# Performance work log

Measured on AMD Instinct MI355X. Metric: run time of the kernel, lower is better.

## Reference

```python
import jax, jax.numpy as jnp
import numpy as np

NUM_HEADS = 12
HEAD_SIZE = 64
N_EMBED = 768
SEQ_LEN = 2048
BATCH = 4


def setup_inputs() -> dict:
    key = jax.random.key(0)
    ks = jax.random.split(key, 7)
    s = 0.02
    x = jax.random.normal(ks[0], (BATCH, SEQ_LEN, N_EMBED), dtype=jnp.float32)
    # per-head bias-free q/k/v projections: [H, E, D]
    Wq = jax.random.normal(ks[1], (NUM_HEADS, N_EMBED, HEAD_SIZE), dtype=jnp.float32) * s
    Wk = jax.random.normal(ks[2], (NUM_HEADS, N_EMBED, HEAD_SIZE), dtype=jnp.float32) * s
    Wv = jax.random.normal(ks[3], (NUM_HEADS, N_EMBED, HEAD_SIZE), dtype=jnp.float32) * s
    # output projection: Linear(num_heads*head_size, n_embed)
    Wp = jax.random.normal(ks[4], (NUM_HEADS * HEAD_SIZE, N_EMBED), dtype=jnp.float32) * s
    bp = jax.random.normal(ks[5], (N_EMBED,), dtype=jnp.float32) * s
    return {"x": x, "Wq": Wq, "Wk": Wk, "Wv": Wv, "Wp": Wp, "bp": bp}


def reference(x, Wq, Wk, Wv, Wp, bp):
    B, S, E = x.shape
    scale = HEAD_SIZE ** -0.5
    # project all heads at once: [B,H,S,D]
    q = jnp.einsum("bse,hed->bhsd", x, Wq)
    k = jnp.einsum("bse,hed->bhsd", x, Wk)
    v = jnp.einsum("bse,hed->bhsd", x, Wv)
    # scaled dot-product scores [B,H,S,S] with causal mask
    scores = jnp.einsum("bhsd,bhtd->bhst", q, k) * scale
    causal = jnp.tril(jnp.ones((S, S), dtype=bool))
    scores = jnp.where(causal[None, None, :, :], scores, jnp.finfo(scores.dtype).min)
    attn = jax.nn.softmax(scores, axis=-1)
    out = jnp.einsum("bhst,bhtd->bhsd", attn, v)
    # concat heads along feature dim: [B,S,H*D]
    out = out.transpose(0, 2, 1, 3).reshape(B, S, NUM_HEADS * HEAD_SIZE)
    # final projection (dropout rate = 0.0)
    return out @ Wp + bp
```

## Files before the change

kernel.cpp:

```cpp
#include <hip/hip_runtime.h>
#include <hip/hip_bf16.h>


typedef __attribute__((ext_vector_type(8))) short bf16x8;
typedef __attribute__((ext_vector_type(4))) float f32x4;
typedef __attribute__((ext_vector_type(16))) float f32x16;
typedef __attribute__((ext_vector_type(4))) uint u32x4;

#define OFF_WT   6291456
#define OFF_WPT  8060928
#define OFF_QKV  8650752
#define OFF_AO   27525120

#define SCALE_LOG2E 0.1803368801111204f

__device__ inline ushort f2bf(float f) {
  __hip_bfloat16 h = __float2bfloat16(f);
  return *reinterpret_cast<ushort*>(&h);
}
__device__ inline uint cvt_pk(float lo, float hi) {
  uint r;
  asm("v_cvt_pk_bf16_f32 %0, %1, %2" : "=v"(r) : "v"(lo), "v"(hi));
  return r;
}

__global__ __launch_bounds__(256) void transpose_w(const float* __restrict__ src,
                                                   ushort* __restrict__ dst,
                                                   int Edim, int Ddim) {
  __shared__ ushort tile[64][130];
  int mat = blockIdx.y;
  int ntd = Ddim >> 6;
  int te = blockIdx.x / ntd, td = blockIdx.x % ntd;
  size_t base = (size_t)mat * Edim * Ddim;
  int t = threadIdx.x;
#pragma unroll
  for (int i = 0; i < 16; i++) {
    int idx = i * 256 + t;
    int r = idx >> 6, c = idx & 63;
    tile[r][c] = f2bf(src[base + (size_t)(te * 64 + r) * Ddim + td * 64 + c]);
  }
  __syncthreads();
#pragma unroll
  for (int i = 0; i < 16; i++) {
    int idx = i * 256 + t;
    int c = idx >> 6, r = idx & 63;
    dst[base + (size_t)(td * 64 + c) * Edim + te * 64 + r] = tile[r][c];
  }
}

__global__ __launch_bounds__(256) void gemm_qkv(const float* __restrict__ X,
                                                const ushort* __restrict__ Wt,
                                                ushort* __restrict__ qkv,
                                                uint* __restrict__ vtg) {
  __shared__ ushort Alds[128 * 40];
  __shared__ ushort Blds[64 * 40];
  int mb = blockIdx.x, nb = blockIdx.y;
  int t = threadIdx.x, w = t >> 6, lane = t & 63, lo = lane & 15, g = lane >> 4;
  const ushort* Wb = Wt + (size_t)nb * 49152;
  f32x4 acc[2][4];
#pragma unroll
  for (int qi = 0; qi < 2; qi++)
#pragma unroll
    for (int n = 0; n < 4; n++) acc[qi][n] = (f32x4){0.f, 0.f, 0.f, 0.f};
  int r = t >> 2, c4 = t & 3;
  for (int e0 = 0; e0 < 768; e0 += 32) {
#pragma unroll
    for (int i = 0; i < 2; i++) {
      const float* src = &X[(size_t)(mb * 128 + i * 64 + r) * 768 + e0 + c4 * 8];
      float4 f0 = *(const float4*)src;
      float4 f1 = *(const float4*)(src + 4);
      u32x4 pk = {cvt_pk(f0.x, f0.y), cvt_pk(f0.z, f0.w),
                  cvt_pk(f1.x, f1.y), cvt_pk(f1.z, f1.w)};
      *(bf16x8*)&Alds[(i * 64 + r) * 40 + c4 * 8] = __builtin_bit_cast(bf16x8, pk);
    }
    *(bf16x8*)&Blds[r * 40 + c4 * 8] =
        *(const bf16x8*)&Wb[(size_t)r * 768 + e0 + c4 * 8];
    __syncthreads();
    bf16x8 a0 = *(const bf16x8*)&Alds[(w * 32 + lo) * 40 + g * 8];
    bf16x8 a1 = *(const bf16x8*)&Alds[(w * 32 + 16 + lo) * 40 + g * 8];
#pragma unroll
    for (int n = 0; n < 4; n++) {
      bf16x8 b = *(const bf16x8*)&Blds[(n * 16 + lo) * 40 + g * 8];
      acc[0][n] = __builtin_amdgcn_mfma_f32_16x16x32_bf16(a0, b, acc[0][n], 0, 0, 0);
      acc[1][n] = __builtin_amdgcn_mfma_f32_16x16x32_bf16(a1, b, acc[1][n], 0, 0, 0);
    }
    __syncthreads();
  }
  int ty = nb / 12, h = nb % 12;
  if (ty < 2) {
#pragma unroll
    for (int qi = 0; qi < 2; qi++)
#pragma unroll
      for (int n = 0; n < 4; n++) {
        int d = n * 16 + lo;
#pragma unroll
        for (int rr = 0; rr < 4; rr++) {
          int m = mb * 128 + w * 32 + qi * 16 + g * 4 + rr;
          int b = m >> 11, s = m & 2047;
          qkv[(size_t)ty * 6291456 + (size_t)(b * 12 + h) * 131072 + (size_t)s * 64 + d] =
              f2bf(acc[qi][n][rr]);
        }
      }
  } else {
#pragma unroll
    for (int qi = 0; qi < 2; qi++)
#pragma unroll
      for (int n = 0; n < 4; n++) {
        int d = n * 16 + lo;
#pragma unroll
        for (int rr = 0; rr < 4; rr += 2) {
          int m = mb * 128 + w * 32 + qi * 16 + g * 4 + rr;
          int b = m >> 11, s = m & 2047;
          uint pk = cvt_pk(acc[qi][n][rr], acc[qi][n][rr + 1]);
          vtg[(size_t)(b * 12 + h) * 65536 + (s >> 6) * 2048 + d * 32 + ((s & 63) >> 1)] = pk;
        }
      }
  }
}

__global__ __launch_bounds__(256, 3) void attn_fwd(const ushort* __restrict__ Qg,
                                                   const ushort* __restrict__ Kg,
                                                   const uint* __restrict__ Vtg,
                                                   ushort* __restrict__ ao) {
  __shared__ ushort Ksh[2][64 * 72];
  __shared__ uint Vsh[2][64 * 36];
  int x = blockIdx.x;
  int head = x % 48;
  int qb = 15 - x / 48;
  int T = 2 * qb + 2;
  int t = threadIdx.x, w = t >> 6, q31 = t & 31, hi = (t & 63) >> 5;
  const ushort* Q = Qg + (size_t)head * 131072;
  const ushort* K = Kg + (size_t)head * 131072;
  const uint* V = Vtg + (size_t)head * 65536;
  int qstart = qb * 128 + 32 * w;
  int qg = qstart + q31;
  bf16x8 qf[4];
#pragma unroll
  for (int s = 0; s < 4; s++)
    qf[s] = *(const bf16x8*)&Q[(size_t)qg * 64 + s * 16 + hi * 8];
  bf16x8 ones;
#pragma unroll
  for (int i = 0; i < 8; i++) ones[i] = (short)0x3F80;
  f32x16 oacc[2], lacc;
#pragma unroll
  for (int r = 0; r < 16; r++) { oacc[0][r] = 0.f; oacc[1][r] = 0.f; lacc[r] = 0.f; }
  int sr = t >> 3, sc = t & 7;
  bf16x8 kreg[2];
  u32x4 vreg[2];
#pragma unroll
  for (int i = 0; i < 2; i++) {
    kreg[i] = *(const bf16x8*)&K[(size_t)(i * 32 + sr) * 64 + sc * 8];
    vreg[i] = *(const u32x4*)&V[(i * 32 + sr) * 32 + sc * 4];
  }
#pragma unroll
  for (int i = 0; i < 2; i++) {
    *(bf16x8*)&Ksh[0][(i * 32 + sr) * 72 + sc * 8] = kreg[i];
    *(u32x4*)&Vsh[0][(i * 32 + sr) * 36 + sc * 4] = vreg[i];
  }
  for (int kb = 0; kb < T; kb++) {
    __syncthreads();
    if (kb + 1 < T) {
      int t1 = (kb + 1) * 64;
#pragma unroll
      for (int i = 0; i < 2; i++) {
        kreg[i] = *(const bf16x8*)&K[(size_t)(t1 + i * 32 + sr) * 64 + sc * 8];
        vreg[i] = *(const u32x4*)&V[(kb + 1) * 2048 + (i * 32 + sr) * 32 + sc * 4];
      }
    }
    int t0 = kb * 64;
    if (t0 <= qstart + 31) {
      const ushort* Kb = Ksh[kb & 1];
      const uint* Vb = Vsh[kb & 1];
      bool act1 = (t0 + 32 <= qstart + 31);
      f32x16 st0, st1;
#pragma unroll
      for (int r = 0; r < 16; r++) { st0[r] = 0.f; st1[r] = 0.f; }
#pragma unroll
      for (int s = 0; s < 4; s++) {
        bf16x8 kf = *(const bf16x8*)&Kb[q31 * 72 + s * 16 + hi * 8];
        st0 = __builtin_amdgcn_mfma_f32_32x32x16_bf16(kf, qf[s], st0, 0, 0, 0);
      }
      if (act1) {
#pragma unroll
        for (int s = 0; s < 4; s++) {
          bf16x8 kf = *(const bf16x8*)&Kb[(32 + q31) * 72 + s * 16 + hi * 8];
          st1 = __builtin_amdgcn_mfma_f32_32x32x16_bf16(kf, qf[s], st1, 0, 0, 0);
        }
      }
      if (t0 + 31 > qstart) {
        int base = t0 - qstart;
#pragma unroll
        for (int r = 0; r < 16; r++) {
          int crow = (r & 3) + 8 * (r >> 2) + 4 * hi;
          if (base + crow > q31) st0[r] = -3e38f;
        }
      }
      if (act1 && (t0 + 63 > qstart)) {
        int base = t0 + 32 - qstart;
#pragma unroll
        for (int r = 0; r < 16; r++) {
          int crow = (r & 3) + 8 * (r >> 2) + 4 * hi;
          if (base + crow > q31) st1[r] = -3e38f;
        }
      }
#pragma unroll
      for (int r = 0; r < 16; r++)
        st0[r] = __builtin_amdgcn_exp2f(st0[r] * SCALE_LOG2E);
      if (act1) {
#pragma unroll
        for (int r = 0; r < 16; r++)
          st1[r] = __builtin_amdgcn_exp2f(st1[r] * SCALE_LOG2E);
      }
      int ns = act1 ? 4 : 2;
      bf16x8 paf[4];
#pragma unroll
      for (int s = 0; s < 4; s++) {
        if (s < ns) {
          const f32x16& sv = (s < 2) ? st0 : st1;
          int rb = (s & 1) * 8;
          uint a = cvt_pk(sv[rb + 0], sv[rb + 1]);
          uint b2 = cvt_pk(sv[rb + 2], sv[rb + 3]);
          uint c = cvt_pk(sv[rb + 4], sv[rb + 5]);
          uint d = cvt_pk(sv[rb + 6], sv[rb + 7]);
          asm volatile("v_permlane32_swap_b32 %0, %1" : "+v"(a), "+v"(c));
          asm volatile("v_permlane32_swap_b32 %0, %1" : "+v"(b2), "+v"(d));
          u32x4 u4 = {a, b2, c, d};
          paf[s] = __builtin_bit_cast(bf16x8, u4);
        }
      }
#pragma unroll
      for (int s = 0; s < 4; s++) {
        if (s < ns) {
          lacc = __builtin_amdgcn_mfma_f32_32x32x16_bf16(paf[s], ones, lacc, 0, 0, 0);
#pragma unroll
          for (int dt = 0; dt < 2; dt++) {
            bf16x8 vf = *(const bf16x8*)&Vb[(dt * 32 + q31) * 36 + s * 8 + hi * 4];
            oacc[dt] = __builtin_amdgcn_mfma_f32_32x32x16_bf16(paf[s], vf, oacc[dt], 0, 0, 0);
          }
        }
      }
    }
    if (kb + 1 < T) {
      int b2 = (kb + 1) & 1;
#pragma unroll
      for (int i = 0; i < 2; i++) {
        *(bf16x8*)&Ksh[b2][(i * 32 + sr) * 72 + sc * 8] = kreg[i];
        *(u32x4*)&Vsh[b2][(i * 32 + sr) * 36 + sc * 4] = vreg[i];
      }
    }
  }
  int hh = head % 12, bb = head / 12;
#pragma unroll
  for (int dt = 0; dt < 2; dt++)
#pragma unroll
    for (int r = 0; r < 16; r++) {
      int qr = qstart + (r & 3) + 8 * (r >> 2) + 4 * hi;
      ao[(size_t)(bb * 2048 + qr) * 768 + hh * 64 + dt * 32 + q31] =
          f2bf(oacc[dt][r] / lacc[r]);
    }
}

__global__ __launch_bounds__(256) void gemm_out(const ushort* __restrict__ A,
                                                const ushort* __restrict__ Bt,
                                                const float* __restrict__ bias,
                                                float* __restrict__ out) {
  __shared__ ushort Alds[128 * 40];
  __shared__ ushort Blds[64 * 40];
  int mb = blockIdx.x, nb = blockIdx.y;
  int t = threadIdx.x, w = t >> 6, lane = t & 63, lo = lane & 15, g = lane >> 4;
  const ushort* Bb = Bt + (size_t)nb * 49152;
  f32x4 acc[2][4];
#pragma unroll
  for (int qi = 0; qi < 2; qi++)
#pragma unroll
    for (int n = 0; n < 4; n++) acc[qi][n] = (f32x4){0.f, 0.f, 0.f, 0.f};
  int r = t >> 2, c4 = t & 3;
  for (int e0 = 0; e0 < 768; e0 += 32) {
#pragma unroll
    for (int i = 0; i < 2; i++)
      *(bf16x8*)&Alds[(i * 64 + r) * 40 + c4 * 8] =
          *(const bf16x8*)&A[(size_t)(mb * 128 + i * 64 + r) * 768 + e0 + c4 * 8];
    *(bf16x8*)&Blds[r * 40 + c4 * 8] =
        *(const bf16x8*)&Bb[(size_t)r * 768 + e0 + c4 * 8];
    __syncthreads();
    bf16x8 a0 = *(const bf16x8*)&Alds[(w * 32 + lo) * 40 + g * 8];
    bf16x8 a1 = *(const bf16x8*)&Alds[(w * 32 + 16 + lo) * 40 + g * 8];
#pragma unroll
    for (int n = 0; n < 4; n++) {
      bf16x8 b = *(const bf16x8*)&Blds[(n * 16 + lo) * 40 + g * 8];
      acc[0][n] = __builtin_amdgcn_mfma_f32_16x16x32_bf16(a0, b, acc[0][n], 0, 0, 0);
      acc[1][n] = __builtin_amdgcn_mfma_f32_16x16x32_bf16(a1, b, acc[1][n], 0, 0, 0);
    }
    __syncthreads();
  }
#pragma unroll
  for (int qi = 0; qi < 2; qi++)
#pragma unroll
    for (int n = 0; n < 4; n++) {
      int col = nb * 64 + n * 16 + lo;
      float bv = bias[col];
#pragma unroll
      for (int rr = 0; rr < 4; rr++) {
        int m = mb * 128 + w * 32 + qi * 16 + g * 4 + rr;
        out[(size_t)m * 768 + col] = acc[qi][n][rr] + bv;
      }
    }
}

extern "C" void kernel_launch(void* const* d_in, const int* in_sizes, int n_in,
                              void* d_out, int out_size, void* d_ws, size_t ws_size,
                              hipStream_t stream) {
  const float* x  = (const float*)d_in[0];
  const float* Wq = (const float*)d_in[1];
  const float* Wk = (const float*)d_in[2];
  const float* Wv = (const float*)d_in[3];
  const float* Wp = (const float*)d_in[4];
  const float* bp = (const float*)d_in[5];
  float* out = (float*)d_out;
  ushort* ws = (ushort*)d_ws;

  ushort* wt  = ws + OFF_WT;
  ushort* wpt = ws + OFF_WPT;
  ushort* qkv = ws + OFF_QKV;
  uint*   vt  = (uint*)(ws + OFF_QKV + 2 * 6291456);
  ushort* ao  = ws + OFF_AO;

  transpose_w<<<dim3(12, 12), 256, 0, stream>>>(Wq, wt + 0 * 589824, 768, 64);
  transpose_w<<<dim3(12, 12), 256, 0, stream>>>(Wk, wt + 1 * 589824, 768, 64);
  transpose_w<<<dim3(12, 12), 256, 0, stream>>>(Wv, wt + 2 * 589824, 768, 64);
  transpose_w<<<dim3(144, 1), 256, 0, stream>>>(Wp, wpt, 768, 768);

  gemm_qkv<<<dim3(64, 36), 256, 0, stream>>>(x, wt, qkv, vt);
  attn_fwd<<<dim3(768), 256, 0, stream>>>(qkv, qkv + 6291456, vt, ao);
  gemm_out<<<dim3(64, 12), 256, 0, stream>>>(ao, wpt, bp, out);
}
```

Measured before the change: 149.5 us.

## Use larger register tiles, direct-to-LDS swizzled loads, and pre-converted bf16 input in GEMMs

A separate kernel now converts x to bf16 before the QKV projection. Both GEMMs then load tiles with global_load_lds straight into XOR-swizzled shared memory, replacing the padded LDS staging. Each wave now computes a 64x64 output tile of 4x4 MFMA fragments instead of 32x64. That doubles the QKV block's N tile to 128, and gemm_out drops to 128 threads. The goal is more operand reuse per LDS read and fewer conversion and copy instructions, at the cost of an extra pass over x, higher register pressure and fewer blocks.

After: 144.4 us. -3.4%, faster.

```diff
diff --git a/kernel.cpp b/kernel.cpp
--- a/kernel.cpp
+++ b/kernel.cpp
@@ -7,6 +7,7 @@
 typedef __attribute__((ext_vector_type(16))) float f32x16;
 typedef __attribute__((ext_vector_type(4))) uint u32x4;
 
+#define OFF_XB   0
 #define OFF_WT   6291456
 #define OFF_WPT  8060928
 #define OFF_QKV  8650752
@@ -22,6 +23,20 @@
   uint r;
   asm("v_cvt_pk_bf16_f32 %0, %1, %2" : "=v"(r) : "v"(lo), "v"(hi));
   return r;
+}
+#define GLOAD16(g, l)                                                              \
+  __builtin_amdgcn_global_load_lds(                                                \
+      (const __attribute__((address_space(1))) uint*)(g),                          \
+      (__attribute__((address_space(3))) uint*)(l), 16, 0, 0)
+
+__global__ __launch_bounds__(256) void cvt_bf16(const float* __restrict__ src,
+                                                ushort* __restrict__ dst, int n8) {
+  int i = blockIdx.x * 256 + threadIdx.x;
+  if (i >= n8) return;
+  float4 a = *(const float4*)&src[(size_t)i * 8];
+  float4 b = *(const float4*)&src[(size_t)i * 8 + 4];
+  u32x4 pk = {cvt_pk(a.x, a.y), cvt_pk(a.z, a.w), cvt_pk(b.x, b.y), cvt_pk(b.z, b.w)};
+  *(bf16x8*)&dst[(size_t)i * 8] = __builtin_bit_cast(bf16x8, pk);
 }
 
 __global__ __launch_bounds__(256) void transpose_w(const float* __restrict__ src,
@@ -48,70 +63,77 @@
   }
 }
 
-__global__ __launch_bounds__(256) void gemm_qkv(const float* __restrict__ X,
+__device__ inline uint swz(uint row) { return (row + (row >> 2)) & 3; }
+
+__global__ __launch_bounds__(256) void gemm_qkv(const ushort* __restrict__ X,
                                                 const ushort* __restrict__ Wt,
                                                 ushort* __restrict__ qkv,
                                                 uint* __restrict__ vtg) {
-  __shared__ ushort Alds[128 * 40];
-  __shared__ ushort Blds[64 * 40];
+  __shared__ ushort Ash[128 * 32];
+  __shared__ ushort Bsh[128 * 32];
   int mb = blockIdx.x, nb = blockIdx.y;
   int t = threadIdx.x, w = t >> 6, lane = t & 63, lo = lane & 15, g = lane >> 4;
-  const ushort* Wb = Wt + (size_t)nb * 49152;
-  f32x4 acc[2][4];
-#pragma unroll
-  for (int qi = 0; qi < 2; qi++)
-#pragma unroll
-    for (int n = 0; n < 4; n++) acc[qi][n] = (f32x4){0.f, 0.f, 0.f, 0.f};
-  int r = t >> 2, c4 = t & 3;
+  int wr = w >> 1, wc = w & 1;
+  const ushort* Ab = X + (size_t)mb * 128 * 768;
+  const ushort* Bb = Wt + (size_t)nb * 128 * 768;
+  f32x4 acc[4][4];
+#pragma unroll
+  for (int fi = 0; fi < 4; fi++)
+#pragma unroll
+    for (int fj = 0; fj < 4; fj++) acc[fi][fj] = (f32x4){0.f, 0.f, 0.f, 0.f};
+  uint rsw = swz(lo) << 4;
   for (int e0 = 0; e0 < 768; e0 += 32) {
 #pragma unroll
-    for (int i = 0; i < 2; i++) {
-      const float* src = &X[(size_t)(mb * 128 + i * 64 + r) * 768 + e0 + c4 * 8];
-      float4 f0 = *(const float4*)src;
-      float4 f1 = *(const float4*)(src + 4);
-      u32x4 pk = {cvt_pk(f0.x, f0.y), cvt_pk(f0.z, f0.w),
-                  cvt_pk(f1.x, f1.y), cvt_pk(f1.z, f1.w)};
-      *(bf16x8*)&Alds[(i * 64 + r) * 40 + c4 * 8] = __builtin_bit_cast(bf16x8, pk);
-    }
-    *(bf16x8*)&Blds[r * 40 + c4 * 8] =
-        *(const bf16x8*)&Wb[(size_t)r * 768 + e0 + c4 * 8];
-    __syncthreads();
-    bf16x8 a0 = *(const bf16x8*)&Alds[(w * 32 + lo) * 40 + g * 8];
-    bf16x8 a1 = *(const bf16x8*)&Alds[(w * 32 + 16 + lo) * 40 + g * 8];
-#pragma unroll
-    for (int n = 0; n < 4; n++) {
-      bf16x8 b = *(const bf16x8*)&Blds[(n * 16 + lo) * 40 + g * 8];
-      acc[0][n] = __builtin_amdgcn_mfma_f32_16x16x32_bf16(a0, b, acc[0][n], 0, 0, 0);
-      acc[1][n] = __builtin_amdgcn_mfma_f32_16x16x32_bf16(a1, b, acc[1][n], 0, 0, 0);
-    }
-    __syncthreads();
-  }
-  int ty = nb / 12, h = nb % 12;
+    for (int j = 0; j < 2; j++) {
+      uint ci = w * 128 + j * 64 + lane;
+      uint row = ci >> 2, c = ci & 3;
+      uint sc = (c ^ swz(row)) << 4;
+      GLOAD16((const char*)(Ab + (size_t)row * 768 + e0) + sc, Ash + (w * 128 + j * 64) * 8);
+      GLOAD16((const char*)(Bb + (size_t)row * 768 + e0) + sc, Bsh + (w * 128 + j * 64) * 8);
+    }
+    __syncthreads();
+    bf16x8 af[4], bf[4];
+#pragma unroll
+    for (int fi = 0; fi < 4; fi++) {
+      int arow = wr * 64 + fi * 16 + lo;
+      af[fi] = *(const bf16x8*)((const char*)Ash + arow * 64 + (((g << 4) ^ rsw)));
+      int brow = wc * 64 + fi * 16 + lo;
+      bf[fi] = *(const bf16x8*)((const char*)Bsh + brow * 64 + (((g << 4) ^ rsw)));
+    }
+#pragma unroll
+    for (int fi = 0; fi < 4; fi++)
+#pragma unroll
+      for (int fj = 0; fj < 4; fj++)
+        acc[fi][fj] = __builtin_amdgcn_mfma_f32_16x16x32_bf16(af[fi], bf[fj], acc[fi][fj], 0, 0, 0);
+    __syncthreads();
+  }
+  int mat = nb * 2 + wc;
+  int ty = mat / 12, h = mat % 12;
   if (ty < 2) {
 #pragma unroll
-    for (int qi = 0; qi < 2; qi++)
-#pragma unroll
-      for (int n = 0; n < 4; n++) {
-        int d = n * 16 + lo;
+    for (int fi = 0; fi < 4; fi++)
+#pragma unroll
+      for (int fj = 0; fj < 4; fj++) {
+        int d = fj * 16 + lo;
 #pragma unroll
         for (int rr = 0; rr < 4; rr++) {
-          int m = mb * 128 + w * 32 + qi * 16 + g * 4 + rr;
+          int m = mb * 128 + wr * 64 + fi * 16 + g * 4 + rr;
           int b = m >> 11, s = m & 2047;
           qkv[(size_t)ty * 6291456 + (size_t)(b * 12 + h) * 131072 + (size_t)s * 64 + d] =
-              f2bf(acc[qi][n][rr]);
+              f2bf(acc[fi][fj][rr]);
         }
       }
   } else {
 #pragma unroll
-    for (int qi = 0; qi < 2; qi++)
-#pragma unroll
-      for (int n = 0; n < 4; n++) {
-        int d = n * 16 + lo;
+    for (int fi = 0; fi < 4; fi++)
+#pragma unroll
+      for (int fj = 0; fj < 4; fj++) {
+        int d = fj * 16 + lo;
 #pragma unroll
         for (int rr = 0; rr < 4; rr += 2) {
-          int m = mb * 128 + w * 32 + qi * 16 + g * 4 + rr;
+          int m = mb * 128 + wr * 64 + fi * 16 + g * 4 + rr;
           int b = m >> 11, s = m & 2047;
-          uint pk = cvt_pk(acc[qi][n][rr], acc[qi][n][rr + 1]);
+          uint pk = cvt_pk(acc[fi][fj][rr], acc[fi][fj][rr + 1]);
           vtg[(size_t)(b * 12 + h) * 65536 + (s >> 6) * 2048 + d * 32 + ((s & 63) >> 1)] = pk;
         }
       }
@@ -260,51 +282,65 @@
     }
 }
 
-__global__ __launch_bounds__(256) void gemm_out(const ushort* __restrict__ A,
+__global__ __launch_bounds__(128) void gemm_out(const ushort* __restrict__ A,
                                                 const ushort* __restrict__ Bt,
                                                 const float* __restrict__ bias,
                                                 float* __restrict__ out) {
-  __shared__ ushort Alds[128 * 40];
-  __shared__ ushort Blds[64 * 40];
+  __shared__ ushort Ash[128 * 32];
+  __shared__ ushort Bsh[64 * 32];
   int mb = blockIdx.x, nb = blockIdx.y;
   int t = threadIdx.x, w = t >> 6, lane = t & 63, lo = lane & 15, g = lane >> 4;
-  const ushort* Bb = Bt + (size_t)nb * 49152;
-  f32x4 acc[2][4];
-#pragma unroll
-  for (int qi = 0; qi < 2; qi++)
-#pragma unroll
-    for (int n = 0; n < 4; n++) acc[qi][n] = (f32x4){0.f, 0.f, 0.f, 0.f};
-  int r = t >> 2, c4 = t & 3;
+  const ushort* Ab = A + (size_t)mb * 128 * 768;
+  const ushort* Bb = Bt + (size_t)nb * 64 * 768;
+  f32x4 acc[4][4];
+#pragma unroll
+  for (int fi = 0; fi < 4; fi++)
+#pragma unroll
+    for (int fj = 0; fj < 4; fj++) acc[fi][fj] = (f32x4){0.f, 0.f, 0.f, 0.f};
+  uint rsw = swz(lo) << 4;
   for (int e0 = 0; e0 < 768; e0 += 32) {
 #pragma unroll
-    for (int i = 0; i < 2; i++)
-      *(bf16x8*)&Alds[(i * 64 + r) * 40 + c4 * 8] =
-          *(const bf16x8*)&A[(size_t)(mb * 128 + i * 64 + r) * 768 + e0 + c4 * 8];
-    *(bf16x8*)&Blds[r * 40 + c4 * 8] =
-        *(const bf16x8*)&Bb[(size_t)r * 768 + e0 + c4 * 8];
-    __syncthreads();
-    bf16x8 a0 = *(const bf16x8*)&Alds[(w * 32 + lo) * 40 + g * 8];
-    bf16x8 a1 = *(const bf16x8*)&Alds[(w * 32 + 16 + lo) * 40 + g * 8];
-#pragma unroll
-    for (int n = 0; n < 4; n++) {
-      bf16x8 b = *(const bf16x8*)&Blds[(n * 16 + lo) * 40 + g * 8];
-      acc[0][n] = __builtin_amdgcn_mfma_f32_16x16x32_bf16(a0, b, acc[0][n], 0, 0, 0);
-      acc[1][n] = __builtin_amdgcn_mfma_f32_16x16x32_bf16(a1, b, acc[1][n], 0, 0, 0);
-    }
-    __syncthreads();
-  }
-#pragma unroll
-  for (int qi = 0; qi < 2; qi++)
-#pragma unroll
-    for (int n = 0; n < 4; n++) {
-      int col = nb * 64 + n * 16 + lo;
-      float bv = bias[col];
+    for (int j = 0; j < 4; j++) {
+      uint ci = w * 256 + j * 64 + lane;
+      uint row = ci >> 2, c = ci & 3;
+      uint sc = (c ^ swz(row)) << 4;
+      GLOAD16((const char*)(Ab + (size_t)row * 768 + e0) + sc, Ash + (w * 256 + j * 64) * 8);
+    }
+#pragma unroll
+    for (int j = 0; j < 2; j++) {
+      uint ci = w * 128 + j * 64 + lane;
+      uint row = ci >> 2, c = ci & 3;
+      uint sc = (c ^ swz(row)) << 4;
+      GLOAD16((const char*)(Bb + (size_t)row * 768 + e0) + sc, Bsh + (w * 128 + j * 64) * 8);
+    }
+    __syncthreads();
+    bf16x8 af[4], bf[4];
+#pragma unroll
+    for (int fi = 0; fi < 4; fi++) {
+      int arow = w * 64 + fi * 16 + lo;
+      af[fi] = *(const bf16x8*)((const char*)Ash + arow * 64 + ((g << 4) ^ rsw));
+      int brow = fi * 16 + lo;
+      bf[fi] = *(const bf16x8*)((const char*)Bsh + brow * 64 + ((g << 4) ^ rsw));
+    }
+#pragma unroll
+    for (int fi = 0; fi < 4; fi++)
+#pragma unroll
+      for (int fj = 0; fj < 4; fj++)
+        acc[fi][fj] = __builtin_amdgcn_mfma_f32_16x16x32_bf16(af[fi], bf[fj], acc[fi][fj], 0, 0, 0);
+    __syncthreads();
+  }
+#pragma unroll
+  for (int fj = 0; fj < 4; fj++) {
+    int col = nb * 64 + fj * 16 + lo;
+    float bv = bias[col];
+#pragma unroll
+    for (int fi = 0; fi < 4; fi++)
 #pragma unroll
       for (int rr = 0; rr < 4; rr++) {
-        int m = mb * 128 + w * 32 + qi * 16 + g * 4 + rr;
-        out[(size_t)m * 768 + col] = acc[qi][n][rr] + bv;
-      }
-    }
+        int m = mb * 128 + w * 64 + fi * 16 + g * 4 + rr;
+        out[(size_t)m * 768 + col] = acc[fi][fj][rr] + bv;
+      }
+  }
 }
 
 extern "C" void kernel_launch(void* const* d_in, const int* in_sizes, int n_in,
@@ -319,18 +355,20 @@
   float* out = (float*)d_out;
   ushort* ws = (ushort*)d_ws;
 
+  ushort* xb  = ws + OFF_XB;
   ushort* wt  = ws + OFF_WT;
   ushort* wpt = ws + OFF_WPT;
   ushort* qkv = ws + OFF_QKV;
   uint*   vt  = (uint*)(ws + OFF_QKV + 2 * 6291456);
   ushort* ao  = ws + OFF_AO;
 
+  cvt_bf16<<<dim3(3072), 256, 0, stream>>>(x, xb, 786432);
   transpose_w<<<dim3(12, 12), 256, 0, stream>>>(Wq, wt + 0 * 589824, 768, 64);
   transpose_w<<<dim3(12, 12), 256, 0, stream>>>(Wk, wt + 1 * 589824, 768, 64);
   transpose_w<<<dim3(12, 12), 256, 0, stream>>>(Wv, wt + 2 * 589824, 768, 64);
   transpose_w<<<dim3(144, 1), 256, 0, stream>>>(Wp, wpt, 768, 768);
 
-  gemm_qkv<<<dim3(64, 36), 256, 0, stream>>>(x, wt, qkv, vt);
+  gemm_qkv<<<dim3(64, 18), 256, 0, stream>>>(xb, wt, qkv, vt);
   attn_fwd<<<dim3(768), 256, 0, stream>>>(qkv, qkv + 6291456, vt, ao);
-  gemm_out<<<dim3(64, 12), 256, 0, stream>>>(ao, wpt, bp, out);
-}
+  gemm_out<<<dim3(64, 12), 128, 0, stream>>>(ao, wpt, bp, out);
+}
```
